# Performance work log

Hardware: AMD Instinct MI355X
Metric: run time of the kernel (lower is better)

## Reference

```python
import jax, jax.numpy as jnp
import numpy as np
import math

N = 100000   # nodes
E = 500000   # edges
IN_C = 128
EDGE_D = 64
HEADS = 4
OUT_C = 32
HC = HEADS * OUT_C  # 128


def setup_inputs() -> dict:
    key = jax.random.key(0)
    ks = jax.random.split(key, 12)
    s_in = 1.0 / math.sqrt(IN_C)
    s_e = 1.0 / math.sqrt(EDGE_D)
    return {
        "x": jax.random.normal(ks[0], (N, IN_C), jnp.float32),
        "edge_index": jax.random.randint(ks[1], (2, E), 0, N, dtype=jnp.int32),
        "edge_attr": jax.random.normal(ks[2], (E, EDGE_D), jnp.float32),
        "Wq": jax.random.uniform(ks[3], (HC, IN_C), jnp.float32, -s_in, s_in),
        "bq": jax.random.uniform(ks[4], (HC,), jnp.float32, -s_in, s_in),
        "Wk": jax.random.uniform(ks[5], (HC, IN_C), jnp.float32, -s_in, s_in),
        "bk": jax.random.uniform(ks[6], (HC,), jnp.float32, -s_in, s_in),
        "Wv": jax.random.uniform(ks[7], (HC, IN_C), jnp.float32, -s_in, s_in),
        "bv": jax.random.uniform(ks[8], (HC,), jnp.float32, -s_in, s_in),
        "We": jax.random.uniform(ks[9], (HC, EDGE_D), jnp.float32, -s_e, s_e),
        "Ws": jax.random.uniform(ks[10], (HC, IN_C), jnp.float32, -s_in, s_in),
        "bs": jax.random.uniform(ks[11], (HC,), jnp.float32, -s_in, s_in),
    }


def reference(x, edge_index, edge_attr, Wq, bq, Wk, bk, Wv, bv, We, Ws, bs):
    src = edge_index[0]
    dst = edge_index[1]
    x_i = x[dst]                       # [E, IN_C] target-node feats
    x_j = x[src]                       # [E, IN_C] source-node feats

    e = (edge_attr @ We.T).reshape(E, HEADS, OUT_C)
    q = (x_i @ Wq.T + bq).reshape(E, HEADS, OUT_C)
    k = (x_j @ Wk.T + bk).reshape(E, HEADS, OUT_C) + e

    alpha = jnp.sum(q * k, axis=-1) / jnp.sqrt(jnp.float32(OUT_C))  # [E, H]
    # Faithful to the source: GLOBAL per-column max (not per-segment), then
    # segment-sum of exponentials over destination nodes.
    m = jnp.max(alpha, axis=0)                                      # [H]
    exp_a = jnp.exp(alpha - m)                                      # [E, H]
    denom = jax.ops.segment_sum(exp_a, dst, num_segments=N)         # [N, H]
    alpha = exp_a / (denom[dst] + 1e-16)                            # [E, H]

    v = (x_j @ Wv.T + bv).reshape(E, HEADS, OUT_C) + e
    msg = v * alpha[:, :, None]                                     # [E, H, C]

    out = jax.ops.segment_sum(msg.reshape(E, HC), dst, num_segments=N)  # [N, HC]
    out = out + (x @ Ws.T + bs)
    return out
```

## Files before the change

### kernel.cpp

```cpp
#include <hip/hip_runtime.h>
#include <hip/hip_bf16.h>
#include <math.h>

#define N_NODES 100000
#define N_EDGES 500000
#define M0 8.0f
#define INV_SQRT32 0.17677669529663687f
#define NB_SCAN 98

static __device__ __forceinline__ unsigned short f2bf(float f) {
    __hip_bfloat16 h = __float2bfloat16(f);
    return *(unsigned short*)&h;
}

__global__ __launch_bounds__(256) void node_proj_kernel(
    const float* __restrict__ x,
    const float* __restrict__ Wq, const float* __restrict__ bq,
    const float* __restrict__ Wk, const float* __restrict__ bk,
    const float* __restrict__ Wv, const float* __restrict__ bv,
    const float* __restrict__ Ws, const float* __restrict__ bs,
    float* __restrict__ Qn, float* __restrict__ Kn, float* __restrict__ Vn,
    float* __restrict__ out)
{
    __shared__ float xsT[32][132];
    __shared__ float wtT[32][132];

    const int t = threadIdx.x;
    const int rb = blockIdx.x >> 2;
    const int cb = blockIdx.x & 3;
    const long r0 = (long)rb * 128;

    const float* W    = (cb == 0) ? Wq : (cb == 1) ? Wk : (cb == 2) ? Wv : Ws;
    const float* bias = (cb == 0) ? bq : (cb == 1) ? bk : (cb == 2) ? bv : bs;
    float* dstp       = (cb == 0) ? Qn : (cb == 1) ? Kn : (cb == 2) ? Vn : out;

    const int tx = t & 15;
    const int ty = t >> 4;

    float acc[8][8];
#pragma unroll
    for (int i = 0; i < 8; ++i)
#pragma unroll
        for (int j = 0; j < 8; ++j) acc[i][j] = 0.f;

    for (int kc = 0; kc < 128; kc += 32) {
        __syncthreads();
        for (int i = t; i < 1024; i += 256) {
            const int r = i >> 3;
            const int c4 = (i & 7) * 4;
            const long row = r0 + r;
            float4 xv = (row < N_NODES) ? *(const float4*)&x[row * 128 + kc + c4]
                                        : make_float4(0.f, 0.f, 0.f, 0.f);
            xsT[c4 + 0][r] = xv.x; xsT[c4 + 1][r] = xv.y;
            xsT[c4 + 2][r] = xv.z; xsT[c4 + 3][r] = xv.w;
            float4 wv = *(const float4*)&W[r * 128 + kc + c4];
            wtT[c4 + 0][r] = wv.x; wtT[c4 + 1][r] = wv.y;
            wtT[c4 + 2][r] = wv.z; wtT[c4 + 3][r] = wv.w;
        }
        __syncthreads();
#pragma unroll 4
        for (int k = 0; k < 32; ++k) {
            const float4 a0 = *(const float4*)&xsT[k][ty * 8];
            const float4 a1 = *(const float4*)&xsT[k][ty * 8 + 4];
            const float4 b0 = *(const float4*)&wtT[k][tx * 4];
            const float4 b1 = *(const float4*)&wtT[k][64 + tx * 4];
            const float a[8] = {a0.x, a0.y, a0.z, a0.w, a1.x, a1.y, a1.z, a1.w};
            const float b[8] = {b0.x, b0.y, b0.z, b0.w, b1.x, b1.y, b1.z, b1.w};
#pragma unroll
            for (int i = 0; i < 8; ++i)
#pragma unroll
                for (int j = 0; j < 8; ++j)
                    acc[i][j] = fmaf(a[i], b[j], acc[i][j]);
        }
    }

    float bias0[4], bias1[4];
#pragma unroll
    for (int j = 0; j < 4; ++j) {
        bias0[j] = bias[tx * 4 + j];
        bias1[j] = bias[64 + tx * 4 + j];
    }

#pragma unroll
    for (int i = 0; i < 8; ++i) {
        const long row = r0 + ty * 8 + i;
        if (row < N_NODES) {
            float4 o0 = make_float4(acc[i][0] + bias0[0], acc[i][1] + bias0[1],
                                    acc[i][2] + bias0[2], acc[i][3] + bias0[3]);
            float4 o1 = make_float4(acc[i][4] + bias1[0], acc[i][5] + bias1[1],
                                    acc[i][6] + bias1[2], acc[i][7] + bias1[3]);
            *(float4*)&dstp[row * 128 + tx * 4] = o0;
            *(float4*)&dstp[row * 128 + 64 + tx * 4] = o1;
        }
    }
}

__global__ __launch_bounds__(256) void ee_gemm_kernel(
    const float* __restrict__ ea, const float* __restrict__ We,
    unsigned short* __restrict__ Ee)
{
    __shared__ float easT[32][132];
    __shared__ float wesT[32][132];

    const int t = threadIdx.x;
    const long e0 = (long)blockIdx.x * 128;
    const int tx = t & 15;
    const int ty = t >> 4;

    float acc[8][8];
#pragma unroll
    for (int i = 0; i < 8; ++i)
#pragma unroll
        for (int j = 0; j < 8; ++j) acc[i][j] = 0.f;

    for (int kc = 0; kc < 64; kc += 32) {
        __syncthreads();
        for (int i = t; i < 1024; i += 256) {
            const int r = i >> 3;
            const int c4 = (i & 7) * 4;
            const long e = e0 + r;
            float4 av = (e < N_EDGES) ? *(const float4*)&ea[e * 64 + kc + c4]
                                      : make_float4(0.f, 0.f, 0.f, 0.f);
            easT[c4 + 0][r] = av.x; easT[c4 + 1][r] = av.y;
            easT[c4 + 2][r] = av.z; easT[c4 + 3][r] = av.w;
            float4 wv = *(const float4*)&We[r * 64 + kc + c4];
            wesT[c4 + 0][r] = wv.x; wesT[c4 + 1][r] = wv.y;
            wesT[c4 + 2][r] = wv.z; wesT[c4 + 3][r] = wv.w;
        }
        __syncthreads();
#pragma unroll 4
        for (int k = 0; k < 32; ++k) {
            const float4 a0 = *(const float4*)&easT[k][ty * 8];
            const float4 a1 = *(const float4*)&easT[k][ty * 8 + 4];
            const float4 b0 = *(const float4*)&wesT[k][tx * 4];
            const float4 b1 = *(const float4*)&wesT[k][64 + tx * 4];
            const float a[8] = {a0.x, a0.y, a0.z, a0.w, a1.x, a1.y, a1.z, a1.w};
            const float b[8] = {b0.x, b0.y, b0.z, b0.w, b1.x, b1.y, b1.z, b1.w};
#pragma unroll
            for (int i = 0; i < 8; ++i)
#pragma unroll
                for (int j = 0; j < 8; ++j)
                    acc[i][j] = fmaf(a[i], b[j], acc[i][j]);
        }
    }

#pragma unroll
    for (int i = 0; i < 8; ++i) {
        const long e = e0 + ty * 8 + i;
        if (e < N_EDGES) {
            ushort4 u0, u1;
            u0.x = f2bf(acc[i][0]); u0.y = f2bf(acc[i][1]);
            u0.z = f2bf(acc[i][2]); u0.w = f2bf(acc[i][3]);
            u1.x = f2bf(acc[i][4]); u1.y = f2bf(acc[i][5]);
            u1.z = f2bf(acc[i][6]); u1.w = f2bf(acc[i][7]);
            *(ushort4*)&Ee[e * 128 + tx * 4] = u0;
            *(ushort4*)&Ee[e * 128 + 64 + tx * 4] = u1;
        }
    }
}

__global__ __launch_bounds__(256) void csr_hist_kernel(
    const int* __restrict__ ei, int* __restrict__ cursor)
{
    const int e = blockIdx.x * 256 + threadIdx.x;
    if (e >= N_EDGES) return;
    atomicAdd(&cursor[ei[N_EDGES + e]], 1);
}

__global__ __launch_bounds__(256) void csr_scan_part_kernel(
    const int* __restrict__ deg, int* __restrict__ bsum)
{
    __shared__ int red[256];
    const int t = threadIdx.x;
    const int i0 = blockIdx.x * 1024 + t * 4;
    int s = 0;
#pragma unroll
    for (int j = 0; j < 4; ++j) {
        const int n = i0 + j;
        if (n < N_NODES) s += deg[n];
    }
    red[t] = s;
    __syncthreads();
    for (int o = 128; o > 0; o >>= 1) {
        if (t < o) red[t] += red[t + o];
        __syncthreads();
    }
    if (t == 0) bsum[blockIdx.x] = red[0];
}

__global__ void csr_scan_top_kernel(int* __restrict__ bsum, int* __restrict__ csr_off)
{
    if (threadIdx.x == 0 && blockIdx.x == 0) {
        int run = 0;
        for (int b = 0; b < NB_SCAN; ++b) {
            const int v = bsum[b];
            bsum[b] = run;
            run += v;
        }
        csr_off[N_NODES] = run;
    }
}

__global__ __launch_bounds__(256) void csr_scan_final_kernel(
    const int* __restrict__ bsum, int* __restrict__ cursor,
    int* __restrict__ csr_off)
{
    __shared__ int ts[256];
    const int t = threadIdx.x;
    const int i0 = blockIdx.x * 1024 + t * 4;
    int d[4];
    int s = 0;
#pragma unroll
    for (int j = 0; j < 4; ++j) {
        const int n = i0 + j;
        d[j] = (n < N_NODES) ? cursor[n] : 0;
        s += d[j];
    }
    ts[t] = s;
    __syncthreads();
    for (int o = 1; o < 256; o <<= 1) {
        int v = (t >= o) ? ts[t - o] : 0;
        __syncthreads();
        ts[t] += v;
        __syncthreads();
    }
    int run = bsum[blockIdx.x] + ts[t] - s;
#pragma unroll
    for (int j = 0; j < 4; ++j) {
        const int n = i0 + j;
        if (n < N_NODES) {
            csr_off[n] = run;
            cursor[n] = run;
            run += d[j];
        }
    }
}

__global__ __launch_bounds__(256) void csr_fill_kernel(
    const int* __restrict__ ei, int* __restrict__ cursor,
    int* __restrict__ csr_eid, int* __restrict__ csr_src)
{
    const int e = blockIdx.x * 256 + threadIdx.x;
    if (e >= N_EDGES) return;
    const int dst = ei[N_EDGES + e];
    const int pos = atomicAdd(&cursor[dst], 1);
    csr_eid[pos] = e;
    csr_src[pos] = ei[e];
}

__global__ __launch_bounds__(256) void fused_attn_kernel(
    const int* __restrict__ csr_off, const int* __restrict__ csr_eid,
    const int* __restrict__ csr_src, const unsigned short* __restrict__ Ee,
    const float* __restrict__ Qn, const float* __restrict__ Kn,
    const float* __restrict__ Vn, float* __restrict__ out)
{
    const int lane = threadIdx.x & 63;
    const int l2 = lane * 2;
    const long n = (long)blockIdx.x * 4 + (threadIdx.x >> 6);

    const int off0 = csr_off[n];
    const int off1 = csr_off[n + 1];
    const float2 q = *(const float2*)&Qn[n * 128 + l2];
    float2 acc = *(const float2*)&out[n * 128 + l2];

    float dsum = 0.f;
    for (int base = off0; base < off1; base += 64) {
        const int cnt = min(64, off1 - base);
        int eid = 0, src = 0;
        if (base + lane < off1) {
            eid = csr_eid[base + lane];
            src = csr_src[base + lane];
        }
        for (int j = 0; j < cnt; ++j) {
            const long e = __shfl(eid, j, 64);
            const long s = __shfl(src, j, 64);
            const unsigned u = *(const unsigned*)&Ee[e * 128 + l2];
            const float2 k = *(const float2*)&Kn[s * 128 + l2];
            float p = q.x * (k.x + __uint_as_float(u << 16)) +
                      q.y * (k.y + __uint_as_float(u & 0xffff0000u));
#pragma unroll
            for (int o = 1; o < 16; o <<= 1) p += __shfl_xor(p, o, 64);
            dsum += __expf(p * INV_SQRT32 - M0);
        }
    }
    const float rd = 1.f / (dsum + 1e-16f);

    for (int base = off0; base < off1; base += 64) {
        const int cnt = min(64, off1 - base);
        int eid = 0, src = 0;
        if (base + lane < off1) {
            eid = csr_eid[base + lane];
            src = csr_src[base + lane];
        }
        for (int j = 0; j < cnt; ++j) {
            const long e = __shfl(eid, j, 64);
            const long s = __shfl(src, j, 64);
            const unsigned u = *(const unsigned*)&Ee[e * 128 + l2];
            const float2 k = *(const float2*)&Kn[s * 128 + l2];
            const float ea0 = __uint_as_float(u << 16);
            const float ea1 = __uint_as_float(u & 0xffff0000u);
            float p = q.x * (k.x + ea0) + q.y * (k.y + ea1);
#pragma unroll
            for (int o = 1; o < 16; o <<= 1) p += __shfl_xor(p, o, 64);
            const float an = __expf(p * INV_SQRT32 - M0) * rd;
            const float2 v = *(const float2*)&Vn[s * 128 + l2];
            acc.x = fmaf(v.x + ea0, an, acc.x);
            acc.y = fmaf(v.y + ea1, an, acc.y);
        }
    }
    *(float2*)&out[n * 128 + l2] = acc;
}

extern "C" void kernel_launch(void* const* d_in, const int* in_sizes, int n_in,
                              void* d_out, int out_size, void* d_ws, size_t ws_size,
                              hipStream_t stream)
{
    const float* x  = (const float*)d_in[0];
    const int*   ei = (const int*)d_in[1];
    const float* ea = (const float*)d_in[2];
    const float* Wq = (const float*)d_in[3];
    const float* bq = (const float*)d_in[4];
    const float* Wk = (const float*)d_in[5];
    const float* bk = (const float*)d_in[6];
    const float* Wv = (const float*)d_in[7];
    const float* bv = (const float*)d_in[8];
    const float* We = (const float*)d_in[9];
    const float* Ws = (const float*)d_in[10];
    const float* bs = (const float*)d_in[11];
    float* out = (float*)d_out;

    float* ws = (float*)d_ws;
    float* Qn = ws;
    float* Kn = ws + 12800000;
    float* Vn = ws + 25600000;
    int* csr_off = (int*)(ws + 38400000);
    int* cursor  = (int*)(ws + 38500004);
    int* csr_eid = (int*)(ws + 38600004);
    int* csr_src = (int*)(ws + 39100004);
    int* bsum    = (int*)(ws + 39600004);
    unsigned short* Ee = (unsigned short*)((char*)d_ws + 163200032);

    hipMemsetAsync(cursor, 0, N_NODES * sizeof(int), stream);

    node_proj_kernel<<<782 * 4, 256, 0, stream>>>(x, Wq, bq, Wk, bk, Wv, bv, Ws, bs,
                                                  Qn, Kn, Vn, out);
    ee_gemm_kernel<<<(N_EDGES + 127) / 128, 256, 0, stream>>>(ea, We, Ee);

    csr_hist_kernel<<<(N_EDGES + 255) / 256, 256, 0, stream>>>(ei, cursor);
    csr_scan_part_kernel<<<NB_SCAN, 256, 0, stream>>>(cursor, bsum);
    csr_scan_top_kernel<<<1, 64, 0, stream>>>(bsum, csr_off);
    csr_scan_final_kernel<<<NB_SCAN, 256, 0, stream>>>(bsum, cursor, csr_off);
    csr_fill_kernel<<<(N_EDGES + 255) / 256, 256, 0, stream>>>(ei, cursor, csr_eid, csr_src);

    fused_attn_kernel<<<25000, 256, 0, stream>>>(csr_off, csr_eid, csr_src, Ee,
                                                 Qn, Kn, Vn, out);
}
```

Measured before the change: 676.0 us.

## Move node and edge projection GEMMs to split-bf16 MFMA

Replaces the FP32 FMA tiled GEMMs for the node projections (Q/K/V/skip) and the edge-attribute projection with MFMA bf16 kernels. Each operand is split into high and low bf16 parts, and three MFMAs per tile keep accuracy close to FP32. A small prep kernel converts the weights once per call. The node kernel now stages one x tile in swizzled LDS and loops over all four weight matrices, so x is read once instead of four times. The trade-off is extra conversion work, more LDS use, and stores of 16-wide rows in scalar form, which are less coalesced than the old float4 stores.

```diff
diff --git a/kernel.cpp b/kernel.cpp
--- a/kernel.cpp
+++ b/kernel.cpp
@@ -8,153 +8,249 @@
 #define INV_SQRT32 0.17677669529663687f
 #define NB_SCAN 98
 
+typedef __attribute__((ext_vector_type(8))) short bf16x8;
+typedef __attribute__((ext_vector_type(4))) float f32x4;
+typedef __attribute__((ext_vector_type(8))) unsigned short us8;
+
 static __device__ __forceinline__ unsigned short f2bf(float f) {
     __hip_bfloat16 h = __float2bfloat16(f);
     return *(unsigned short*)&h;
 }
 
-__global__ __launch_bounds__(256) void node_proj_kernel(
+__global__ __launch_bounds__(256) void prep_w_kernel(
+    const float* __restrict__ Wq, const float* __restrict__ Wk,
+    const float* __restrict__ Wv, const float* __restrict__ Ws,
+    const float* __restrict__ We,
+    unsigned short* __restrict__ WBh, unsigned short* __restrict__ WBl,
+    unsigned short* __restrict__ WEh, unsigned short* __restrict__ WEl)
+{
+    const int i = blockIdx.x * 256 + threadIdx.x;
+    float v;
+    unsigned short *ph, *pl;
+    int idx;
+    if (i < 65536) {
+        const int p = i >> 14;
+        const float* W = (p == 0) ? Wq : (p == 1) ? Wk : (p == 2) ? Wv : Ws;
+        v = W[i & 16383];
+        ph = WBh; pl = WBl; idx = i;
+    } else if (i < 73728) {
+        idx = i - 65536;
+        v = We[idx];
+        ph = WEh; pl = WEl;
+    } else {
+        return;
+    }
+    const unsigned short h = f2bf(v);
+    ph[idx] = h;
+    pl[idx] = f2bf(v - __uint_as_float((unsigned)h << 16));
+}
+
+__global__ __launch_bounds__(256) void node_proj_mfma(
     const float* __restrict__ x,
-    const float* __restrict__ Wq, const float* __restrict__ bq,
-    const float* __restrict__ Wk, const float* __restrict__ bk,
-    const float* __restrict__ Wv, const float* __restrict__ bv,
-    const float* __restrict__ Ws, const float* __restrict__ bs,
+    const unsigned short* __restrict__ WBh, const unsigned short* __restrict__ WBl,
+    const float* __restrict__ bq, const float* __restrict__ bk,
+    const float* __restrict__ bv, const float* __restrict__ bs,
     float* __restrict__ Qn, float* __restrict__ Kn, float* __restrict__ Vn,
     float* __restrict__ out)
 {
-    __shared__ float xsT[32][132];
-    __shared__ float wtT[32][132];
+    __shared__ __align__(16) unsigned short xh[64 * 128];
+    __shared__ __align__(16) unsigned short xl[64 * 128];
+    __shared__ __align__(16) unsigned short wh[128 * 64];
+    __shared__ __align__(16) unsigned short wl[128 * 64];
 
     const int t = threadIdx.x;
-    const int rb = blockIdx.x >> 2;
-    const int cb = blockIdx.x & 3;
-    const long r0 = (long)rb * 128;
-
-    const float* W    = (cb == 0) ? Wq : (cb == 1) ? Wk : (cb == 2) ? Wv : Ws;
-    const float* bias = (cb == 0) ? bq : (cb == 1) ? bk : (cb == 2) ? bv : bs;
-    float* dstp       = (cb == 0) ? Qn : (cb == 1) ? Kn : (cb == 2) ? Vn : out;
-
-    const int tx = t & 15;
-    const int ty = t >> 4;
-
-    float acc[8][8];
-#pragma unroll
-    for (int i = 0; i < 8; ++i)
-#pragma unroll
-        for (int j = 0; j < 8; ++j) acc[i][j] = 0.f;
-
-    for (int kc = 0; kc < 128; kc += 32) {
-        __syncthreads();
-        for (int i = t; i < 1024; i += 256) {
-            const int r = i >> 3;
-            const int c4 = (i & 7) * 4;
-            const long row = r0 + r;
-            float4 xv = (row < N_NODES) ? *(const float4*)&x[row * 128 + kc + c4]
-                                        : make_float4(0.f, 0.f, 0.f, 0.f);
-            xsT[c4 + 0][r] = xv.x; xsT[c4 + 1][r] = xv.y;
-            xsT[c4 + 2][r] = xv.z; xsT[c4 + 3][r] = xv.w;
-            float4 wv = *(const float4*)&W[r * 128 + kc + c4];
-            wtT[c4 + 0][r] = wv.x; wtT[c4 + 1][r] = wv.y;
-            wtT[c4 + 2][r] = wv.z; wtT[c4 + 3][r] = wv.w;
-        }
-        __syncthreads();
-#pragma unroll 4
-        for (int k = 0; k < 32; ++k) {
-            const float4 a0 = *(const float4*)&xsT[k][ty * 8];
-            const float4 a1 = *(const float4*)&xsT[k][ty * 8 + 4];
-            const float4 b0 = *(const float4*)&wtT[k][tx * 4];
-            const float4 b1 = *(const float4*)&wtT[k][64 + tx * 4];
-            const float a[8] = {a0.x, a0.y, a0.z, a0.w, a1.x, a1.y, a1.z, a1.w};
-            const float b[8] = {b0.x, b0.y, b0.z, b0.w, b1.x, b1.y, b1.z, b1.w};
-#pragma unroll
-            for (int i = 0; i < 8; ++i)
-#pragma unroll
-                for (int j = 0; j < 8; ++j)
-                    acc[i][j] = fmaf(a[i], b[j], acc[i][j]);
-        }
-    }
-
-    float bias0[4], bias1[4];
-#pragma unroll
-    for (int j = 0; j < 4; ++j) {
-        bias0[j] = bias[tx * 4 + j];
-        bias1[j] = bias[64 + tx * 4 + j];
-    }
-
-#pragma unroll
-    for (int i = 0; i < 8; ++i) {
-        const long row = r0 + ty * 8 + i;
-        if (row < N_NODES) {
-            float4 o0 = make_float4(acc[i][0] + bias0[0], acc[i][1] + bias0[1],
-                                    acc[i][2] + bias0[2], acc[i][3] + bias0[3]);
-            float4 o1 = make_float4(acc[i][4] + bias1[0], acc[i][5] + bias1[1],
-                                    acc[i][6] + bias1[2], acc[i][7] + bias1[3]);
-            *(float4*)&dstp[row * 128 + tx * 4] = o0;
-            *(float4*)&dstp[row * 128 + 64 + tx * 4] = o1;
-        }
-    }
-}
-
-__global__ __launch_bounds__(256) void ee_gemm_kernel(
-    const float* __restrict__ ea, const float* __restrict__ We,
+    const long r0 = (long)blockIdx.x * 64;
+    const int lane = t & 63;
+    const int wid = t >> 6;
+    const int fr = lane & 15;
+    const int fq = lane >> 4;
+
+    for (int i = t; i < 64 * 32; i += 256) {
+        const int r = i >> 5;
+        const int s = i & 31;
+        const long row = r0 + r;
+        float4 v = (row < N_NODES) ? *(const float4*)&x[row * 128 + s * 4]
+                                   : make_float4(0.f, 0.f, 0.f, 0.f);
+        const unsigned short h0 = f2bf(v.x), h1 = f2bf(v.y),
+                             h2 = f2bf(v.z), h3 = f2bf(v.w);
+        ushort4 hv, lv;
+        hv.x = h0; hv.y = h1; hv.z = h2; hv.w = h3;
+        lv.x = f2bf(v.x - __uint_as_float((unsigned)h0 << 16));
+        lv.y = f2bf(v.y - __uint_as_float((unsigned)h1 << 16));
+        lv.z = f2bf(v.z - __uint_as_float((unsigned)h2 << 16));
+        lv.w = f2bf(v.w - __uint_as_float((unsigned)h3 << 16));
+        const int di = r * 128 + ((s * 4) ^ ((r & 7) << 3));
+        *(ushort4*)&xh[di] = hv;
+        *(ushort4*)&xl[di] = lv;
+    }
+
+    for (int p = 0; p < 4; ++p) {
+        const float* bias = (p == 0) ? bq : (p == 1) ? bk : (p == 2) ? bv : bs;
+        float* dst        = (p == 0) ? Qn : (p == 1) ? Kn : (p == 2) ? Vn : out;
+
+        f32x4 acc[4][2];
+#pragma unroll
+        for (int m = 0; m < 4; ++m)
+#pragma unroll
+            for (int n = 0; n < 2; ++n) acc[m][n] = (f32x4){0.f, 0.f, 0.f, 0.f};
+
+        for (int kc = 0; kc < 2; ++kc) {
+            __syncthreads();
+            for (int i = t; i < 1024; i += 256) {
+                const int r = i >> 3;
+                const int s = i & 7;
+                const int gi = p * 16384 + r * 128 + kc * 64 + s * 8;
+                const int di = r * 64 + ((s * 8) ^ ((r & 7) << 3));
+                *(us8*)&wh[di] = *(const us8*)&WBh[gi];
+                *(us8*)&wl[di] = *(const us8*)&WBl[gi];
+            }
+            __syncthreads();
+
+#pragma unroll
+            for (int ks = 0; ks < 2; ++ks) {
+                const int kx = kc * 64 + ks * 32 + fq * 8;
+                const int kw = ks * 32 + fq * 8;
+                bf16x8 ah[4], al[4], bh[2], bl[2];
+#pragma unroll
+                for (int m = 0; m < 4; ++m) {
+                    const int r = m * 16 + fr;
+                    const int di = r * 128 + (kx ^ ((r & 7) << 3));
+                    ah[m] = *(const bf16x8*)&xh[di];
+                    al[m] = *(const bf16x8*)&xl[di];
+                }
+#pragma unroll
+                for (int n = 0; n < 2; ++n) {
+                    const int r = wid * 32 + n * 16 + fr;
+                    const int di = r * 64 + (kw ^ ((r & 7) << 3));
+                    bh[n] = *(const bf16x8*)&wh[di];
+                    bl[n] = *(const bf16x8*)&wl[di];
+                }
+#pragma unroll
+                for (int m = 0; m < 4; ++m)
+#pragma unroll
+                    for (int n = 0; n < 2; ++n) {
+                        acc[m][n] = __builtin_amdgcn_mfma_f32_16x16x32_bf16(
+                            ah[m], bh[n], acc[m][n], 0, 0, 0);
+                        acc[m][n] = __builtin_amdgcn_mfma_f32_16x16x32_bf16(
+                            ah[m], bl[n], acc[m][n], 0, 0, 0);
+                        acc[m][n] = __builtin_amdgcn_mfma_f32_16x16x32_bf16(
+                            al[m], bh[n], acc[m][n], 0, 0, 0);
+                    }
+            }
+        }
+
+        float bb[2];
+#pragma unroll
+        for (int n = 0; n < 2; ++n) bb[n] = bias[wid * 32 + n * 16 + fr];
+#pragma unroll
+        for (int m = 0; m < 4; ++m) {
+            const long rowb = r0 + m * 16 + fq * 4;
+#pragma unroll
+            for (int j = 0; j < 4; ++j) {
+                if (rowb + j < N_NODES) {
+#pragma unroll
+                    for (int n = 0; n < 2; ++n)
+                        dst[(rowb + j) * 128 + wid * 32 + n * 16 + fr] =
+                            acc[m][n][j] + bb[n];
+                }
+            }
+        }
+    }
+}
+
+__global__ __launch_bounds__(256) void ee_gemm_mfma(
+    const float* __restrict__ ea,
+    const unsigned short* __restrict__ WEh, const unsigned short* __restrict__ WEl,
     unsigned short* __restrict__ Ee)
 {
-    __shared__ float easT[32][132];
-    __shared__ float wesT[32][132];
+    __shared__ __align__(16) unsigned short eh[128 * 64];
+    __shared__ __align__(16) unsigned short el[128 * 64];
+    __shared__ __align__(16) unsigned short wh[128 * 64];
+    __shared__ __align__(16) unsigned short wl[128 * 64];
 
     const int t = threadIdx.x;
     const long e0 = (long)blockIdx.x * 128;
-    const int tx = t & 15;
-    const int ty = t >> 4;
-
-    float acc[8][8];
-#pragma unroll
-    for (int i = 0; i < 8; ++i)
-#pragma unroll
-        for (int j = 0; j < 8; ++j) acc[i][j] = 0.f;
-
-    for (int kc = 0; kc < 64; kc += 32) {
-        __syncthreads();
-        for (int i = t; i < 1024; i += 256) {
-            const int r = i >> 3;
-            const int c4 = (i & 7) * 4;
-            const long e = e0 + r;
-            float4 av = (e < N_EDGES) ? *(const float4*)&ea[e * 64 + kc + c4]
-                                      : make_float4(0.f, 0.f, 0.f, 0.f);
-            easT[c4 + 0][r] = av.x; easT[c4 + 1][r] = av.y;
-            easT[c4 + 2][r] = av.z; easT[c4 + 3][r] = av.w;
-            float4 wv = *(const float4*)&We[r * 64 + kc + c4];
-            wesT[c4 + 0][r] = wv.x; wesT[c4 + 1][r] = wv.y;
-            wesT[c4 + 2][r] = wv.z; wesT[c4 + 3][r] = wv.w;
-        }
-        __syncthreads();
-#pragma unroll 4
-        for (int k = 0; k < 32; ++k) {
-            const float4 a0 = *(const float4*)&easT[k][ty * 8];
-            const float4 a1 = *(const float4*)&easT[k][ty * 8 + 4];
-            const float4 b0 = *(const float4*)&wesT[k][tx * 4];
-            const float4 b1 = *(const float4*)&wesT[k][64 + tx * 4];
-            const float a[8] = {a0.x, a0.y, a0.z, a0.w, a1.x, a1.y, a1.z, a1.w};
-            const float b[8] = {b0.x, b0.y, b0.z, b0.w, b1.x, b1.y, b1.z, b1.w};
-#pragma unroll
-            for (int i = 0; i < 8; ++i)
-#pragma unroll
-                for (int j = 0; j < 8; ++j)
-                    acc[i][j] = fmaf(a[i], b[j], acc[i][j]);
-        }
-    }
-
-#pragma unroll
-    for (int i = 0; i < 8; ++i) {
-        const long e = e0 + ty * 8 + i;
-        if (e < N_EDGES) {
-            ushort4 u0, u1;
-            u0.x = f2bf(acc[i][0]); u0.y = f2bf(acc[i][1]);
-            u0.z = f2bf(acc[i][2]); u0.w = f2bf(acc[i][3]);
-            u1.x = f2bf(acc[i][4]); u1.y = f2bf(acc[i][5]);
-            u1.z = f2bf(acc[i][6]); u1.w = f2bf(acc[i][7]);
-            *(ushort4*)&Ee[e * 128 + tx * 4] = u0;
-            *(ushort4*)&Ee[e * 128 + 64 + tx * 4] = u1;
+    const int lane = t & 63;
+    const int wr = (t >> 6) >> 1;
+    const int wc = (t >> 6) & 1;
+    const int fr = lane & 15;
+    const int fq = lane >> 4;
+
+    for (int i = t; i < 1024; i += 256) {
+        const int r = i >> 3;
+        const int s = i & 7;
+        const int di = r * 64 + ((s * 8) ^ ((r & 7) << 3));
+        *(us8*)&wh[di] = *(const us8*)&WEh[r * 64 + s * 8];
+        *(us8*)&wl[di] = *(const us8*)&WEl[r * 64 + s * 8];
+    }
+    for (int i = t; i < 128 * 16; i += 256) {
+        const int r = i >> 4;
+        const int s = i & 15;
+        const long e = e0 + r;
+        float4 v = (e < N_EDGES) ? *(const float4*)&ea[e * 64 + s * 4]
+                                 : make_float4(0.f, 0.f, 0.f, 0.f);
+        const unsigned short h0 = f2bf(v.x), h1 = f2bf(v.y),
+                             h2 = f2bf(v.z), h3 = f2bf(v.w);
+        ushort4 hv, lv;
+        hv.x = h0; hv.y = h1; hv.z = h2; hv.w = h3;
+        lv.x = f2bf(v.x - __uint_as_float((unsigned)h0 << 16));
+        lv.y = f2bf(v.y - __uint_as_float((unsigned)h1 << 16));
+        lv.z = f2bf(v.z - __uint_as_float((unsigned)h2 << 16));
+        lv.w = f2bf(v.w - __uint_as_float((unsigned)h3 << 16));
+        const int di = r * 64 + ((s * 4) ^ ((r & 7) << 3));
+        *(ushort4*)&eh[di] = hv;
+        *(ushort4*)&el[di] = lv;
+    }
+    __syncthreads();
+
+    f32x4 acc[4][4];
+#pragma unroll
+    for (int m = 0; m < 4; ++m)
+#pragma unroll
+        for (int n = 0; n < 4; ++n) acc[m][n] = (f32x4){0.f, 0.f, 0.f, 0.f};
+
+#pragma unroll
+    for (int ks = 0; ks < 2; ++ks) {
+        const int kk = ks * 32 + fq * 8;
+        bf16x8 ah[4], al[4], bh[4], bl[4];
+#pragma unroll
+        for (int m = 0; m < 4; ++m) {
+            const int r = wr * 64 + m * 16 + fr;
+            const int di = r * 64 + (kk ^ ((r & 7) << 3));
+            ah[m] = *(const bf16x8*)&eh[di];
+            al[m] = *(const bf16x8*)&el[di];
+        }
+#pragma unroll
+        for (int n = 0; n < 4; ++n) {
+            const int r = wc * 64 + n * 16 + fr;
+            const int di = r * 64 + (kk ^ ((r & 7) << 3));
+            bh[n] = *(const bf16x8*)&wh[di];
+            bl[n] = *(const bf16x8*)&wl[di];
+        }
+#pragma unroll
+        for (int m = 0; m < 4; ++m)
+#pragma unroll
+            for (int n = 0; n < 4; ++n) {
+                acc[m][n] = __builtin_amdgcn_mfma_f32_16x16x32_bf16(
+                    ah[m], bh[n], acc[m][n], 0, 0, 0);
+                acc[m][n] = __builtin_amdgcn_mfma_f32_16x16x32_bf16(
+                    ah[m], bl[n], acc[m][n], 0, 0, 0);
+                acc[m][n] = __builtin_amdgcn_mfma_f32_16x16x32_bf16(
+                    al[m], bh[n], acc[m][n], 0, 0, 0);
+            }
+    }
+
+#pragma unroll
+    for (int m = 0; m < 4; ++m) {
+        const long erow = e0 + wr * 64 + m * 16 + fq * 4;
+#pragma unroll
+        for (int j = 0; j < 4; ++j) {
+            if (erow + j < N_EDGES) {
+#pragma unroll
+                for (int n = 0; n < 4; ++n)
+                    Ee[(erow + j) * 128 + wc * 64 + n * 16 + fr] =
+                        f2bf(acc[m][n][j]);
+            }
         }
     }
 }
@@ -338,13 +434,19 @@
     int* csr_eid = (int*)(ws + 38600004);
     int* csr_src = (int*)(ws + 39100004);
     int* bsum    = (int*)(ws + 39600004);
+    unsigned short* WBh = (unsigned short*)(ws + 40000000);
+    unsigned short* WBl = (unsigned short*)(ws + 40050000);
+    unsigned short* WEh = (unsigned short*)(ws + 40100000);
+    unsigned short* WEl = (unsigned short*)(ws + 40110000);
     unsigned short* Ee = (unsigned short*)((char*)d_ws + 163200032);
 
     hipMemsetAsync(cursor, 0, N_NODES * sizeof(int), stream);
 
-    node_proj_kernel<<<782 * 4, 256, 0, stream>>>(x, Wq, bq, Wk, bk, Wv, bv, Ws, bs,
-                                                  Qn, Kn, Vn, out);
-    ee_gemm_kernel<<<(N_EDGES + 127) / 128, 256, 0, stream>>>(ea, We, Ee);
+    prep_w_kernel<<<288, 256, 0, stream>>>(Wq, Wk, Wv, Ws, We, WBh, WBl, WEh, WEl);
+
+    node_proj_mfma<<<1563, 256, 0, stream>>>(x, WBh, WBl, bq, bk, bv, bs,
+                                             Qn, Kn, Vn, out);
+    ee_gemm_mfma<<<3907, 256, 0, stream>>>(ea, WEh, WEl, Ee);
 
     csr_hist_kernel<<<(N_EDGES + 255) / 256, 256, 0, stream>>>(ei, cursor);
     csr_scan_part_kernel<<<NB_SCAN, 256, 0, stream>>>(cursor, bsum);
```

Measured after the change: 644.3 us. 4.7% less time.
